# Optimization experiments

Hardware: AMD Instinct MI355X
Metric: run time of the kernel (lower is better)

Reference implementation:

```python
import jax, jax.numpy as jnp
import numpy as np

LN_EPS = 1e-5
NORM_EPS = 1e-12  # F.normalize eps


def _l2norm(x):
    # torch F.normalize(p=2, dim=-1): x / max(||x||, eps)
    n = jnp.sqrt(jnp.sum(x * x, axis=-1, keepdims=True))
    return x / jnp.maximum(n, NORM_EPS)


def setup_inputs() -> dict:
    key = jax.random.key(0)
    D, R, H = 256, 32, 64  # d_model, rank, d_model//4
    B, C, P = 32, 64, 96
    ks = jax.random.split(key, 16)
    s = 0.05
    return {
        "x": jax.random.normal(ks[0], (B * C, P, D), jnp.float32),
        "ln_gamma": jnp.ones((D,), jnp.float32),
        "ln_beta": jnp.zeros((D,), jnp.float32),
        "Wd": jax.random.normal(ks[1], (D, R), jnp.float32) * s,
        "bd": jax.random.normal(ks[2], (R,), jnp.float32) * s,
        "Wq": jax.random.normal(ks[3], (R, R), jnp.float32) * s,
        "Wk": jax.random.normal(ks[4], (R, R), jnp.float32) * s,
        "Wv": jax.random.normal(ks[5], (R, R), jnp.float32) * s,
        "Wg": jax.random.normal(ks[6], (R, R), jnp.float32) * s,
        "bg": jax.random.normal(ks[7], (R,), jnp.float32) * s,
        "Wu": jax.random.normal(ks[8], (R, D), jnp.float32) * s,
        "bu": jax.random.normal(ks[9], (D,), jnp.float32) * s,
        "W1": jax.random.normal(ks[10], (D, H), jnp.float32) * s,
        "b1": jax.random.normal(ks[11], (H,), jnp.float32) * s,
        "W2": jax.random.normal(ks[12], (H, D), jnp.float32) * s,
        "b2": jnp.full((D,), -5.0, jnp.float32),  # gate_init bias
        "B": B,
        "C": C,
    }


def reference(x, ln_gamma, ln_beta, Wd, bd, Wq, Wk, Wv, Wg, bg, Wu, bu, W1, b1, W2, b2, B, C):
    BC, P, D = x.shape
    # [B*C, P, D] -> [B*P, C, D] channel-mixing layout
    h = x.reshape(B, C, P, D).transpose(0, 2, 1, 3).reshape(B * P, C, D)

    # LayerNorm over D (biased variance, as in torch LayerNorm)
    mu = jnp.mean(h, axis=-1, keepdims=True)
    var = jnp.var(h, axis=-1, keepdims=True)
    h_norm = (h - mu) * jax.lax.rsqrt(var + LN_EPS) * ln_gamma + ln_beta

    # bottleneck projection to rank R
    h_low = h_norm @ Wd + bd  # [BP, C, R]

    # Hydra linear attention: cosine-normalized Q/K, sum-pooled K*V global feature
    Q = _l2norm(h_low @ Wq)
    K = _l2norm(h_low @ Wk)
    V = h_low @ Wv
    global_feat = jnp.sum(K * V, axis=1, keepdims=True)  # [BP, 1, R]
    h_attn = Q * global_feat

    # content gate and up-projection
    gate_c = jax.nn.sigmoid(h_low @ Wg + bg)
    mixed = (h_attn * gate_c) @ Wu + bu  # [BP, C, D]

    # AdaptiveGate: unbiased variance over channel dim (torch .var default ddof=1)
    chan_var = jnp.var(h, axis=1, ddof=1)  # [BP, D]
    gate_logits = jax.nn.gelu(chan_var @ W1 + b1, approximate=False) @ W2 + b2
    gate = jax.nn.sigmoid(gate_logits)[:, None, :]  # [BP, 1, D]

    out = h + gate * mixed
    # back to [B*C, P, D]
    return out.reshape(B, P, C, D).transpose(0, 2, 1, 3).reshape(BC, P, D)
```

## Files before the change

### kernel.cpp

```cpp
#include <hip/hip_runtime.h>
#include <hip/hip_bf16.h>

#define DD 256
#define RR 32
#define CC 64
#define PB 96
#define NT 1024

typedef __attribute__((ext_vector_type(8))) short short8;
typedef __attribute__((ext_vector_type(4))) float f32x4;

__device__ __forceinline__ short f2bf(float f) {
    return __builtin_bit_cast(short, __float2bfloat16(f));
}
__device__ __forceinline__ float b2f(unsigned short s) {
    union { unsigned u; float f; } v; v.u = ((unsigned)s) << 16;
    return v.f;
}

__device__ __forceinline__ int hswz(int c, int d) {
    return c * 256 + (d ^ ((c & 7) << 3));
}
__device__ __forceinline__ int nswz(int r, int k) {
    return r * 32 + (k ^ (((r >> 1) & 3) << 3));
}

__global__ __launch_bounds__(1024, 1)
void prep_kernel(const float* __restrict__ ln_g, const float* __restrict__ ln_b,
                 const float* __restrict__ Wd, const float* __restrict__ bd,
                 const float* __restrict__ Wq, const float* __restrict__ Wk,
                 const float* __restrict__ Wv, const float* __restrict__ Wg,
                 const float* __restrict__ Wu,
                 const float* __restrict__ W1, const float* __restrict__ W2,
                 short* __restrict__ wsWd, short* __restrict__ wsQKVG,
                 short* __restrict__ wsWu, float* __restrict__ wsLN,
                 float* __restrict__ wsW1T, float* __restrict__ wsW2T)
{
    __shared__ float redp[2048];
    const int t = threadIdx.x;
    {
        const int r = t >> 5, dblk = t & 31;
        short8 vv;
        float sa = 0.f, sb = 0.f;
        #pragma unroll
        for (int j = 0; j < 8; ++j) {
            const int d = dblk * 8 + j;
            const float wd = Wd[d * RR + r];
            const float g  = ln_g[d];
            vv[j] = f2bf(g * wd);
            sa += g * wd;
            sb += ln_b[d] * wd;
        }
        *(short8*)&wsWd[r * 256 + ((dblk ^ (r & 7)) << 3)] = vv;
        redp[r * 32 + dblk]        = sa;
        redp[1024 + r * 32 + dblk] = sb;
    }
    if (t < 512) {
        const int m = t >> 7, rr2 = (t >> 2) & 31, kg = t & 3;
        const float* Wm = (m == 0) ? Wq : (m == 1) ? Wk : (m == 2) ? Wv : Wg;
        short8 vv;
        #pragma unroll
        for (int j = 0; j < 8; ++j)
            vv[j] = f2bf(Wm[(kg * 8 + j) * RR + rr2]);
        *(short8*)&wsQKVG[m * 1024 + rr2 * 32 + ((kg ^ ((rr2 >> 1) & 3)) << 3)] = vv;
    }
    {
        const int d = t & 255, kg = t >> 8;
        short8 vv;
        #pragma unroll
        for (int j = 0; j < 8; ++j)
            vv[j] = f2bf(Wu[(kg * 8 + j) * DD + d]);
        *(short8*)&wsWu[d * 32 + ((kg ^ ((d >> 1) & 3)) << 3)] = vv;
    }
    #pragma unroll
    for (int rep = 0; rep < 16; ++rep) {
        const int id = rep * 1024 + t;
        const int j = id >> 8, d = id & 255;
        wsW1T[j * 256 + d] = W1[d * 64 + j];
    }
    #pragma unroll
    for (int rep = 0; rep < 16; ++rep) {
        const int id = rep * 1024 + t;
        const int d = id >> 6, j = id & 63;
        wsW2T[d * 64 + j] = W2[j * 256 + d];
    }
    __syncthreads();
    if (t < 32) {
        float s = 0.f;
        #pragma unroll
        for (int g = 0; g < 32; ++g) s += redp[t * 32 + g];
        wsLN[t] = s;
    } else if (t < 64) {
        const int r = t - 32;
        float s = 0.f;
        #pragma unroll
        for (int g = 0; g < 32; ++g) s += redp[1024 + r * 32 + g];
        wsLN[t] = s + bd[r];
    }
}

__global__ __launch_bounds__(NT, 8)
void hydra_kernel(const float* __restrict__ x,
                  const short* __restrict__ wsWd, const short* __restrict__ wsQKVG,
                  const short* __restrict__ wsWu, const float* __restrict__ wsLN,
                  const float* __restrict__ wsW1T, const float* __restrict__ wsW2T,
                  const float* __restrict__ bg,
                  const float* __restrict__ bu,
                  const float* __restrict__ b1, const float* __restrict__ b2,
                  float* __restrict__ out)
{
    __shared__ short hbf[CC * DD];
    __shared__ short wreg[RR * DD];
    __shared__ short qg[CC * RR];
    __shared__ short lowbuf[CC * RR];
    __shared__ float redA[1024];
    __shared__ float redB[2048];
    __shared__ float redC[1024];
    __shared__ float mu_s[CC], rstd_s[CC];
    __shared__ float cv_s[DD], gate_s[DD];
    __shared__ float hid_s[64];
    __shared__ float ln_a[RR], ln_bv[RR];

    const int t    = threadIdx.x;
    const int lane = t & 63;
    const int w    = t >> 6;
    const int bp   = blockIdx.x;
    const int b    = bp / PB;
    const int p    = bp - b * PB;
    const size_t rowbase = (size_t)(b * CC) * PB * DD + (size_t)p * DD;

    #pragma unroll
    for (int i = 0; i < 4; ++i) {
        const int c = w * 4 + i;
        const float4 v = *(const float4*)(x + rowbase + (size_t)c * (PB * DD) + 4 * lane);
        float s1 = v.x + v.y + v.z + v.w;
        float s2 = v.x * v.x + v.y * v.y + v.z * v.z + v.w * v.w;
        s1 += __shfl_xor(s1, 1, 64); s2 += __shfl_xor(s2, 1, 64);
        s1 += __shfl_xor(s1, 2, 64); s2 += __shfl_xor(s2, 2, 64);
        s1 += __shfl_xor(s1, 4, 64); s2 += __shfl_xor(s2, 4, 64);
        if ((lane & 7) == 0)
            *(float2*)&redC[(c * 8 + (lane >> 3)) * 2] = make_float2(s1, s2);
        ushort4 pk;
        pk.x = (unsigned short)f2bf(v.x); pk.y = (unsigned short)f2bf(v.y);
        pk.z = (unsigned short)f2bf(v.z); pk.w = (unsigned short)f2bf(v.w);
        *(ushort4*)&hbf[hswz(c, 4 * lane)] = pk;
    }
    *(short8*)&wreg[t * 8] = *(const short8*)&wsWd[t * 8];
    if (t < 32)              ln_a[t]       = wsLN[t];
    else if (t < 64)         ln_bv[t - 32] = wsLN[t];
    __syncthreads();

    f32x4 s3acc = {0.f, 0.f, 0.f, 0.f};
    if (w < 8) {
        const int ct = w >> 1, rt = w & 1;
        const int arow = ct * 16 + (lane & 15);
        const int brow = rt * 16 + (lane & 15);
        const int ksub = lane >> 4;
        #pragma unroll
        for (int step = 0; step < 8; ++step) {
            const short8 a  = *(const short8*)&hbf[hswz(arow, step * 32 + ksub * 8)];
            const short8 bf = *(const short8*)&wreg[hswz(brow, step * 32 + ksub * 8)];
            s3acc = __builtin_amdgcn_mfma_f32_16x16x32_bf16(a, bf, s3acc, 0, 0, 0);
        }
    } else {
        const int idx = t - 512;
        const int dp  = idx & 127;
        const int rg  = idx >> 7;
        const int d0  = dp * 2;
        float s1a = 0.f, s1b = 0.f, s2a = 0.f, s2b = 0.f;
        #pragma unroll
        for (int i = 0; i < 16; ++i) {
            const int c = rg * 16 + i;
            const ushort2 u = *(const ushort2*)&hbf[hswz(c, d0)];
            const float va = b2f(u.x), vb = b2f(u.y);
            s1a += va; s2a += va * va;
            s1b += vb; s2b += vb * vb;
        }
        *(float2*)&redB[rg * 256 + d0]        = make_float2(s1a, s1b);
        *(float2*)&redB[1024 + rg * 256 + d0] = make_float2(s2a, s2b);
        if (idx < 64) {
            const int c = idx;
            float s1 = 0.f, s2 = 0.f;
            #pragma unroll
            for (int g = 0; g < 8; ++g) {
                const float2 pr = *(const float2*)&redC[(c * 8 + g) * 2];
                s1 += pr.x; s2 += pr.y;
            }
            const float mu = s1 * (1.f / 256.f);
            mu_s[c]   = mu;
            rstd_s[c] = rsqrtf(s2 * (1.f / 256.f) - mu * mu + 1e-5f);
        }
    }
    __syncthreads();

    if (w < 8) {
        const int ct = w >> 1, rt = w & 1;
        const int col = rt * 16 + (lane & 15);
        const float la = ln_a[col], lb = ln_bv[col];
        #pragma unroll
        for (int i = 0; i < 4; ++i) {
            const int c = ct * 16 + (lane >> 4) * 4 + i;
            const float rs = rstd_s[c];
            const float hl = rs * s3acc[i] - rs * mu_s[c] * la + lb;
            lowbuf[nswz(c, col)] = f2bf(hl);
        }
    } else {
        const int idx = t - 512;
        *(short8*)&wreg[idx * 8] = *(const short8*)&wsQKVG[idx * 8];
    }
    if (t < 256) {
        const float S1 = redB[t] + redB[256 + t] + redB[512 + t] + redB[768 + t];
        const float S2 = redB[1024 + t] + redB[1280 + t] + redB[1536 + t] + redB[1792 + t];
        cv_s[t] = (S2 - S1 * S1 * (1.f / 64.f)) * (1.f / 63.f);
    }
    __syncthreads();

    if (w < 8) {
        const int ct = w >> 1, pair = w & 1;
        const int mA = pair ? 1 : 0;
        const int mB = pair ? 2 : 3;
        const int arow = ct * 16 + (lane & 15);
        const int ksub = lane >> 4;
        const short8 a = *(const short8*)&lowbuf[nswz(arow, ksub * 8)];
        f32x4 aA0 = {0,0,0,0}, aA1 = {0,0,0,0}, aB0 = {0,0,0,0}, aB1 = {0,0,0,0};
        {
            const int br0 = (lane & 15), br1 = 16 + (lane & 15);
            const short8 bA0 = *(const short8*)&wreg[mA * 1024 + nswz(br0, ksub * 8)];
            const short8 bA1 = *(const short8*)&wreg[mA * 1024 + nswz(br1, ksub * 8)];
            const short8 bB0 = *(const short8*)&wreg[mB * 1024 + nswz(br0, ksub * 8)];
            const short8 bB1 = *(const short8*)&wreg[mB * 1024 + nswz(br1, ksub * 8)];
            aA0 = __builtin_amdgcn_mfma_f32_16x16x32_bf16(a, bA0, aA0, 0, 0, 0);
            aA1 = __builtin_amdgcn_mfma_f32_16x16x32_bf16(a, bA1, aA1, 0, 0, 0);
            aB0 = __builtin_amdgcn_mfma_f32_16x16x32_bf16(a, bB0, aB0, 0, 0, 0);
            aB1 = __builtin_amdgcn_mfma_f32_16x16x32_bf16(a, bB1, aB1, 0, 0, 0);
        }
        float qs[4];
        #pragma unroll
        for (int i = 0; i < 4; ++i) {
            float ss = aA0[i] * aA0[i] + aA1[i] * aA1[i];
            ss += __shfl_xor(ss, 1, 64);
            ss += __shfl_xor(ss, 2, 64);
            ss += __shfl_xor(ss, 4, 64);
            ss += __shfl_xor(ss, 8, 64);
            qs[i] = 1.f / fmaxf(sqrtf(ss), 1e-12f);
        }
        const int col0 = (lane & 15), col1 = 16 + (lane & 15);
        if (pair == 0) {
            const float bgv0 = bg[col0], bgv1 = bg[col1];
            #pragma unroll
            for (int i = 0; i < 4; ++i) {
                const int c = ct * 16 + (lane >> 4) * 4 + i;
                const float g0 = 1.f / (1.f + __expf(-(aB0[i] + bgv0)));
                const float g1 = 1.f / (1.f + __expf(-(aB1[i] + bgv1)));
                qg[c * 32 + col0] = f2bf(aA0[i] * qs[i] * g0);
                qg[c * 32 + col1] = f2bf(aA1[i] * qs[i] * g1);
            }
        } else {
            #pragma unroll
            for (int i = 0; i < 4; ++i) {
                const int c = ct * 16 + (lane >> 4) * 4 + i;
                redB[c * 32 + col0] = aA0[i] * qs[i] * aB0[i];
                redB[c * 32 + col1] = aA1[i] * qs[i] * aB1[i];
            }
        }
    } else {
        const int idx = t - 512;
        const int j = idx & 63, dg = idx >> 6;
        const float* w1row = wsW1T + j * 256 + dg * 32;
        float s = 0.f;
        #pragma unroll
        for (int ii = 0; ii < 8; ++ii) {
            const float4 wv = *(const float4*)(w1row + ii * 4);
            const float4 cvv = *(const float4*)&cv_s[dg * 32 + ii * 4];
            s += cvv.x * wv.x + cvv.y * wv.y + cvv.z * wv.z + cvv.w * wv.w;
        }
        redA[dg * 64 + j] = s;
    }
    __syncthreads();

    if (t < 64) {
        float s = b1[t];
        #pragma unroll
        for (int g = 0; g < 8; ++g) s += redA[g * 64 + t];
        hid_s[t] = 0.5f * s * (1.f + erff(s * 0.70710678118654752f));
    }
    if (t >= 256 && t < 512) {
        const int idx = t - 256;
        const int r = idx & 31, g = idx >> 5;
        float s = 0.f;
        #pragma unroll
        for (int i = 0; i < 8; ++i)
            s += redB[(g * 8 + i) * 32 + r];
        redA[512 + g * 32 + r] = s;
    }
    *(short8*)&wreg[t * 8] = *(const short8*)&wsWu[t * 8];
    __syncthreads();

    {
        const int d = t & 255, jg = t >> 8;
        const float* w2row = wsW2T + d * 64 + jg * 16;
        float s = 0.f;
        #pragma unroll
        for (int ii = 0; ii < 4; ++ii) {
            const float4 wv = *(const float4*)(w2row + ii * 4);
            const float4 hv = *(const float4*)&hid_s[jg * 16 + ii * 4];
            s += hv.x * wv.x + hv.y * wv.y + hv.z * wv.z + hv.w * wv.w;
        }
        redB[jg * 256 + d] = s;
    }
    if (t < 256) {
        const int r = t & 31, c0 = t >> 5, c1 = (t >> 5) + 32;
        float gf = 0.f;
        #pragma unroll
        for (int g = 0; g < 8; ++g) gf += redA[512 + g * 32 + r];
        lowbuf[nswz(c0, r)] = f2bf(b2f((unsigned short)qg[c0 * 32 + r]) * gf);
        lowbuf[nswz(c1, r)] = f2bf(b2f((unsigned short)qg[c1 * 32 + r]) * gf);
    }
    __syncthreads();

    {
        const int ct = w & 3, dg = w >> 2;
        const int arow = ct * 16 + (lane & 15);
        const int ksub = lane >> 4;
        const short8 a = *(const short8*)&lowbuf[nswz(arow, ksub * 8)];
        #pragma unroll
        for (int j = 0; j < 4; ++j) {
            const int col = (dg * 4 + j) * 16 + (lane & 15);
            const short8 bf = *(const short8*)&wreg[nswz(col, ksub * 8)];
            f32x4 acc = {0.f, 0.f, 0.f, 0.f};
            acc = __builtin_amdgcn_mfma_f32_16x16x32_bf16(a, bf, acc, 0, 0, 0);
            #pragma unroll
            for (int i = 0; i < 4; ++i) {
                const int c = ct * 16 + (lane >> 4) * 4 + i;
                hbf[hswz(c, col)] = f2bf(acc[i]);
            }
        }
    }
    if (t < 256) {
        const float s = redB[t] + redB[256 + t] + redB[512 + t] + redB[768 + t] + b2[t];
        gate_s[t] = 1.f / (1.f + __expf(-s));
    }
    __syncthreads();

    #pragma unroll
    for (int i = 0; i < 4; ++i) {
        const int c = w * 4 + i;
        const size_t off = rowbase + (size_t)c * (PB * DD) + 4 * lane;
        const float4 xv = *(const float4*)(x + off);
        const ushort4 m = *(const ushort4*)&hbf[hswz(c, 4 * lane)];
        const float4 g4 = *(const float4*)&gate_s[4 * lane];
        const float4 bu4 = *(const float4*)(bu + 4 * lane);
        float4 o;
        o.x = xv.x + g4.x * (b2f(m.x) + bu4.x);
        o.y = xv.y + g4.y * (b2f(m.y) + bu4.y);
        o.z = xv.z + g4.z * (b2f(m.z) + bu4.z);
        o.w = xv.w + g4.w * (b2f(m.w) + bu4.w);
        *(float4*)(out + off) = o;
    }
}

extern "C" void kernel_launch(void* const* d_in, const int* in_sizes, int n_in,
                              void* d_out, int out_size, void* d_ws, size_t ws_size,
                              hipStream_t stream) {
    (void)in_sizes; (void)n_in; (void)out_size; (void)ws_size;
    const float* x    = (const float*)d_in[0];
    const float* ln_g = (const float*)d_in[1];
    const float* ln_b = (const float*)d_in[2];
    const float* Wd   = (const float*)d_in[3];
    const float* bd   = (const float*)d_in[4];
    const float* Wq   = (const float*)d_in[5];
    const float* Wk   = (const float*)d_in[6];
    const float* Wv   = (const float*)d_in[7];
    const float* Wg   = (const float*)d_in[8];
    const float* bg   = (const float*)d_in[9];
    const float* Wu   = (const float*)d_in[10];
    const float* bu   = (const float*)d_in[11];
    const float* W1   = (const float*)d_in[12];
    const float* b1   = (const float*)d_in[13];
    const float* W2   = (const float*)d_in[14];
    const float* b2   = (const float*)d_in[15];
    float* out = (float*)d_out;

    short* wsWd   = (short*)d_ws;
    short* wsQKVG = wsWd + 8192;
    short* wsWu   = wsQKVG + 4096;
    float* wsLN   = (float*)(wsWd + 20480);
    float* wsW1T  = wsLN + 64;
    float* wsW2T  = wsW1T + 16384;

    prep_kernel<<<dim3(1), dim3(1024), 0, stream>>>(
        ln_g, ln_b, Wd, bd, Wq, Wk, Wv, Wg, Wu, W1, W2,
        wsWd, wsQKVG, wsWu, wsLN, wsW1T, wsW2T);
    hydra_kernel<<<dim3(32 * PB), dim3(NT), 0, stream>>>(
        x, wsWd, wsQKVG, wsWu, wsLN, wsW1T, wsW2T, bg, bu, b1, b2, out);
}
```

Before: 169.7 us.

## Pre-pack weights into MFMA fragment order and load B operands from global

The prep kernel now writes Wd, Wq/Wk/Wv/Wg and Wu in per-lane MFMA fragment order. The main kernel reads each B operand with one coalesced short8 global load instead of staging the weights through a 16KB shared buffer. This removes the shared weight buffer and its staging copies and cuts LDS use per block, which may allow more resident blocks. The cost is repeated global/L2 reads of the weights by every block. Those reads should be cache-resident but add latency inside the MFMA loops.

```diff
diff --git a/kernel.cpp b/kernel.cpp
--- a/kernel.cpp
+++ b/kernel.cpp
@@ -32,45 +32,60 @@
                  const float* __restrict__ Wv, const float* __restrict__ Wg,
                  const float* __restrict__ Wu,
                  const float* __restrict__ W1, const float* __restrict__ W2,
-                 short* __restrict__ wsWd, short* __restrict__ wsQKVG,
-                 short* __restrict__ wsWu, float* __restrict__ wsLN,
+                 short* __restrict__ wsF1, short* __restrict__ wsF2,
+                 short* __restrict__ wsF3, float* __restrict__ wsLN,
                  float* __restrict__ wsW1T, float* __restrict__ wsW2T)
 {
     __shared__ float redp[2048];
     const int t = threadIdx.x;
     {
         const int r = t >> 5, dblk = t & 31;
-        short8 vv;
         float sa = 0.f, sb = 0.f;
         #pragma unroll
         for (int j = 0; j < 8; ++j) {
             const int d = dblk * 8 + j;
             const float wd = Wd[d * RR + r];
-            const float g  = ln_g[d];
-            vv[j] = f2bf(g * wd);
-            sa += g * wd;
+            sa += ln_g[d] * wd;
             sb += ln_b[d] * wd;
         }
-        *(short8*)&wsWd[r * 256 + ((dblk ^ (r & 7)) << 3)] = vv;
         redp[r * 32 + dblk]        = sa;
         redp[1024 + r * 32 + dblk] = sb;
     }
+    {
+        const int f = t >> 6, l = t & 63;
+        const int rt = f >> 3, step = f & 7;
+        const int r = rt * 16 + (l & 15);
+        short8 v;
+        #pragma unroll
+        for (int j = 0; j < 8; ++j) {
+            const int d = step * 32 + (l >> 4) * 8 + j;
+            v[j] = f2bf(ln_g[d] * Wd[d * RR + r]);
+        }
+        *(short8*)&wsF1[f * 512 + l * 8] = v;
+    }
     if (t < 512) {
-        const int m = t >> 7, rr2 = (t >> 2) & 31, kg = t & 3;
+        const int f = t >> 6, l = t & 63;
+        const int m = f >> 1, half = f & 1;
         const float* Wm = (m == 0) ? Wq : (m == 1) ? Wk : (m == 2) ? Wv : Wg;
-        short8 vv;
-        #pragma unroll
-        for (int j = 0; j < 8; ++j)
-            vv[j] = f2bf(Wm[(kg * 8 + j) * RR + rr2]);
-        *(short8*)&wsQKVG[m * 1024 + rr2 * 32 + ((kg ^ ((rr2 >> 1) & 3)) << 3)] = vv;
+        const int rout = half * 16 + (l & 15);
+        short8 v;
+        #pragma unroll
+        for (int j = 0; j < 8; ++j) {
+            const int rin = (l >> 4) * 8 + j;
+            v[j] = f2bf(Wm[rin * RR + rout]);
+        }
+        *(short8*)&wsF2[f * 512 + l * 8] = v;
     }
     {
-        const int d = t & 255, kg = t >> 8;
-        short8 vv;
-        #pragma unroll
-        for (int j = 0; j < 8; ++j)
-            vv[j] = f2bf(Wu[(kg * 8 + j) * DD + d]);
-        *(short8*)&wsWu[d * 32 + ((kg ^ ((d >> 1) & 3)) << 3)] = vv;
+        const int f = t >> 6, l = t & 63;
+        const int d = f * 16 + (l & 15);
+        short8 v;
+        #pragma unroll
+        for (int j = 0; j < 8; ++j) {
+            const int r = (l >> 4) * 8 + j;
+            v[j] = f2bf(Wu[r * DD + d]);
+        }
+        *(short8*)&wsF3[f * 512 + l * 8] = v;
     }
     #pragma unroll
     for (int rep = 0; rep < 16; ++rep) {
@@ -101,8 +116,8 @@
 
 __global__ __launch_bounds__(NT, 8)
 void hydra_kernel(const float* __restrict__ x,
-                  const short* __restrict__ wsWd, const short* __restrict__ wsQKVG,
-                  const short* __restrict__ wsWu, const float* __restrict__ wsLN,
+                  const short* __restrict__ wsF1, const short* __restrict__ wsF2,
+                  const short* __restrict__ wsF3, const float* __restrict__ wsLN,
                   const float* __restrict__ wsW1T, const float* __restrict__ wsW2T,
                   const float* __restrict__ bg,
                   const float* __restrict__ bu,
@@ -110,7 +125,6 @@
                   float* __restrict__ out)
 {
     __shared__ short hbf[CC * DD];
-    __shared__ short wreg[RR * DD];
     __shared__ short qg[CC * RR];
     __shared__ short lowbuf[CC * RR];
     __shared__ float redA[1024];
@@ -145,7 +159,6 @@
         pk.z = (unsigned short)f2bf(v.z); pk.w = (unsigned short)f2bf(v.w);
         *(ushort4*)&hbf[hswz(c, 4 * lane)] = pk;
     }
-    *(short8*)&wreg[t * 8] = *(const short8*)&wsWd[t * 8];
     if (t < 32)              ln_a[t]       = wsLN[t];
     else if (t < 64)         ln_bv[t - 32] = wsLN[t];
     __syncthreads();
@@ -154,12 +167,12 @@
     if (w < 8) {
         const int ct = w >> 1, rt = w & 1;
         const int arow = ct * 16 + (lane & 15);
-        const int brow = rt * 16 + (lane & 15);
-        const int ksub = lane >> 4;
+        const int kofs = (lane >> 4) * 8;
+        const short* fB = wsF1 + rt * 8 * 512 + lane * 8;
         #pragma unroll
         for (int step = 0; step < 8; ++step) {
-            const short8 a  = *(const short8*)&hbf[hswz(arow, step * 32 + ksub * 8)];
-            const short8 bf = *(const short8*)&wreg[hswz(brow, step * 32 + ksub * 8)];
+            const short8 bf = *(const short8*)(fB + step * 512);
+            const short8 a  = *(const short8*)&hbf[hswz(arow, step * 32 + kofs)];
             s3acc = __builtin_amdgcn_mfma_f32_16x16x32_bf16(a, bf, s3acc, 0, 0, 0);
         }
     } else {
@@ -204,14 +217,11 @@
             const float hl = rs * s3acc[i] - rs * mu_s[c] * la + lb;
             lowbuf[nswz(c, col)] = f2bf(hl);
         }
-    } else {
-        const int idx = t - 512;
-        *(short8*)&wreg[idx * 8] = *(const short8*)&wsQKVG[idx * 8];
-    }
-    if (t < 256) {
-        const float S1 = redB[t] + redB[256 + t] + redB[512 + t] + redB[768 + t];
-        const float S2 = redB[1024 + t] + redB[1280 + t] + redB[1536 + t] + redB[1792 + t];
-        cv_s[t] = (S2 - S1 * S1 * (1.f / 64.f)) * (1.f / 63.f);
+    } else if (t < 768) {
+        const int d = t - 512;
+        const float S1 = redB[d] + redB[256 + d] + redB[512 + d] + redB[768 + d];
+        const float S2 = redB[1024 + d] + redB[1280 + d] + redB[1536 + d] + redB[1792 + d];
+        cv_s[d] = (S2 - S1 * S1 * (1.f / 64.f)) * (1.f / 63.f);
     }
     __syncthreads();
 
@@ -220,20 +230,17 @@
         const int mA = pair ? 1 : 0;
         const int mB = pair ? 2 : 3;
         const int arow = ct * 16 + (lane & 15);
-        const int ksub = lane >> 4;
-        const short8 a = *(const short8*)&lowbuf[nswz(arow, ksub * 8)];
+        const int kofs = (lane >> 4) * 8;
+        const short8 a = *(const short8*)&lowbuf[nswz(arow, kofs)];
+        const short8 bA0 = *(const short8*)(wsF2 + (mA * 2 + 0) * 512 + lane * 8);
+        const short8 bA1 = *(const short8*)(wsF2 + (mA * 2 + 1) * 512 + lane * 8);
+        const short8 bB0 = *(const short8*)(wsF2 + (mB * 2 + 0) * 512 + lane * 8);
+        const short8 bB1 = *(const short8*)(wsF2 + (mB * 2 + 1) * 512 + lane * 8);
         f32x4 aA0 = {0,0,0,0}, aA1 = {0,0,0,0}, aB0 = {0,0,0,0}, aB1 = {0,0,0,0};
-        {
-            const int br0 = (lane & 15), br1 = 16 + (lane & 15);
-            const short8 bA0 = *(const short8*)&wreg[mA * 1024 + nswz(br0, ksub * 8)];
-            const short8 bA1 = *(const short8*)&wreg[mA * 1024 + nswz(br1, ksub * 8)];
-            const short8 bB0 = *(const short8*)&wreg[mB * 1024 + nswz(br0, ksub * 8)];
-            const short8 bB1 = *(const short8*)&wreg[mB * 1024 + nswz(br1, ksub * 8)];
-            aA0 = __builtin_amdgcn_mfma_f32_16x16x32_bf16(a, bA0, aA0, 0, 0, 0);
-            aA1 = __builtin_amdgcn_mfma_f32_16x16x32_bf16(a, bA1, aA1, 0, 0, 0);
-            aB0 = __builtin_amdgcn_mfma_f32_16x16x32_bf16(a, bB0, aB0, 0, 0, 0);
-            aB1 = __builtin_amdgcn_mfma_f32_16x16x32_bf16(a, bB1, aB1, 0, 0, 0);
-        }
+        aA0 = __builtin_amdgcn_mfma_f32_16x16x32_bf16(a, bA0, aA0, 0, 0, 0);
+        aA1 = __builtin_amdgcn_mfma_f32_16x16x32_bf16(a, bA1, aA1, 0, 0, 0);
+        aB0 = __builtin_amdgcn_mfma_f32_16x16x32_bf16(a, bB0, aB0, 0, 0, 0);
+        aB1 = __builtin_amdgcn_mfma_f32_16x16x32_bf16(a, bB1, aB1, 0, 0, 0);
         float qs[4];
         #pragma unroll
         for (int i = 0; i < 4; ++i) {
@@ -293,7 +300,6 @@
             s += redB[(g * 8 + i) * 32 + r];
         redA[512 + g * 32 + r] = s;
     }
-    *(short8*)&wreg[t * 8] = *(const short8*)&wsWu[t * 8];
     __syncthreads();
 
     {
@@ -321,12 +327,13 @@
     {
         const int ct = w & 3, dg = w >> 2;
         const int arow = ct * 16 + (lane & 15);
-        const int ksub = lane >> 4;
-        const short8 a = *(const short8*)&lowbuf[nswz(arow, ksub * 8)];
+        const int kofs = (lane >> 4) * 8;
+        const short8 a = *(const short8*)&lowbuf[nswz(arow, kofs)];
         #pragma unroll
         for (int j = 0; j < 4; ++j) {
-            const int col = (dg * 4 + j) * 16 + (lane & 15);
-            const short8 bf = *(const short8*)&wreg[nswz(col, ksub * 8)];
+            const int dt = dg * 4 + j;
+            const int col = dt * 16 + (lane & 15);
+            const short8 bf = *(const short8*)(wsF3 + dt * 512 + lane * 8);
             f32x4 acc = {0.f, 0.f, 0.f, 0.f};
             acc = __builtin_amdgcn_mfma_f32_16x16x32_bf16(a, bf, acc, 0, 0, 0);
             #pragma unroll
@@ -381,16 +388,16 @@
     const float* b2   = (const float*)d_in[15];
     float* out = (float*)d_out;
 
-    short* wsWd   = (short*)d_ws;
-    short* wsQKVG = wsWd + 8192;
-    short* wsWu   = wsQKVG + 4096;
-    float* wsLN   = (float*)(wsWd + 20480);
-    float* wsW1T  = wsLN + 64;
-    float* wsW2T  = wsW1T + 16384;
+    short* wsF1  = (short*)d_ws;
+    short* wsF2  = wsF1 + 8192;
+    short* wsF3  = wsF2 + 4096;
+    float* wsLN  = (float*)(wsF1 + 20480);
+    float* wsW1T = wsLN + 64;
+    float* wsW2T = wsW1T + 16384;
 
     prep_kernel<<<dim3(1), dim3(1024), 0, stream>>>(
         ln_g, ln_b, Wd, bd, Wq, Wk, Wv, Wg, Wu, W1, W2,
-        wsWd, wsQKVG, wsWu, wsLN, wsW1T, wsW2T);
+        wsF1, wsF2, wsF3, wsLN, wsW1T, wsW2T);
     hydra_kernel<<<dim3(32 * PB), dim3(NT), 0, stream>>>(
-        x, wsWd, wsQKVG, wsWu, wsLN, wsW1T, wsW2T, bg, bu, b1, b2, out);
-}
+        x, wsF1, wsF2, wsF3, wsLN, wsW1T, wsW2T, bg, bu, b1, b2, out);
+}
```

Result: no change. 171.4 us (+1.0%).

## Fuse gated residual epilogue into the up-projection MFMA and merge gate GEMV

Applied to the files above, without the earlier changes.

The W2 gate GEMV is now done by one thread per output column, bias and sigmoid included, in the same phase as the Q*global scaling. This removes the partial-sum reduction buffer and a barrier. The final output is now written straight from the MFMA accumulators, which removes the staging of mixed in shared memory, another barrier, and the second global read of x. The residual now comes from the bf16 copy of h held in shared memory instead of fp32 x, which lowers output precision. Stores become 16-wide scattered column writes instead of contiguous float4 rows, so write coalescing gets worse.

```diff
diff --git a/kernel.cpp b/kernel.cpp
--- a/kernel.cpp
+++ b/kernel.cpp
@@ -296,18 +296,6 @@
     *(short8*)&wreg[t * 8] = *(const short8*)&wsWu[t * 8];
     __syncthreads();
 
-    {
-        const int d = t & 255, jg = t >> 8;
-        const float* w2row = wsW2T + d * 64 + jg * 16;
-        float s = 0.f;
-        #pragma unroll
-        for (int ii = 0; ii < 4; ++ii) {
-            const float4 wv = *(const float4*)(w2row + ii * 4);
-            const float4 hv = *(const float4*)&hid_s[jg * 16 + ii * 4];
-            s += hv.x * wv.x + hv.y * wv.y + hv.z * wv.z + hv.w * wv.w;
-        }
-        redB[jg * 256 + d] = s;
-    }
     if (t < 256) {
         const int r = t & 31, c0 = t >> 5, c1 = (t >> 5) + 32;
         float gf = 0.f;
@@ -315,6 +303,17 @@
         for (int g = 0; g < 8; ++g) gf += redA[512 + g * 32 + r];
         lowbuf[nswz(c0, r)] = f2bf(b2f((unsigned short)qg[c0 * 32 + r]) * gf);
         lowbuf[nswz(c1, r)] = f2bf(b2f((unsigned short)qg[c1 * 32 + r]) * gf);
+    } else if (t < 512) {
+        const int d = t - 256;
+        const float* w2row = wsW2T + d * 64;
+        float s = b2[d];
+        #pragma unroll
+        for (int ii = 0; ii < 16; ++ii) {
+            const float4 wv = *(const float4*)(w2row + ii * 4);
+            const float4 hv = *(const float4*)&hid_s[ii * 4];
+            s += hv.x * wv.x + hv.y * wv.y + hv.z * wv.z + hv.w * wv.w;
+        }
+        gate_s[d] = 1.f / (1.f + __expf(-s));
     }
     __syncthreads();
 
@@ -329,33 +328,15 @@
             const short8 bf = *(const short8*)&wreg[nswz(col, ksub * 8)];
             f32x4 acc = {0.f, 0.f, 0.f, 0.f};
             acc = __builtin_amdgcn_mfma_f32_16x16x32_bf16(a, bf, acc, 0, 0, 0);
+            const float gt  = gate_s[col];
+            const float buv = bu[col];
             #pragma unroll
             for (int i = 0; i < 4; ++i) {
                 const int c = ct * 16 + (lane >> 4) * 4 + i;
-                hbf[hswz(c, col)] = f2bf(acc[i]);
+                const float xv = b2f((unsigned short)hbf[hswz(c, col)]);
+                out[rowbase + (size_t)c * (PB * DD) + col] = xv + gt * (acc[i] + buv);
             }
         }
-    }
-    if (t < 256) {
-        const float s = redB[t] + redB[256 + t] + redB[512 + t] + redB[768 + t] + b2[t];
-        gate_s[t] = 1.f / (1.f + __expf(-s));
-    }
-    __syncthreads();
-
-    #pragma unroll
-    for (int i = 0; i < 4; ++i) {
-        const int c = w * 4 + i;
-        const size_t off = rowbase + (size_t)c * (PB * DD) + 4 * lane;
-        const float4 xv = *(const float4*)(x + off);
-        const ushort4 m = *(const ushort4*)&hbf[hswz(c, 4 * lane)];
-        const float4 g4 = *(const float4*)&gate_s[4 * lane];
-        const float4 bu4 = *(const float4*)(bu + 4 * lane);
-        float4 o;
-        o.x = xv.x + g4.x * (b2f(m.x) + bu4.x);
-        o.y = xv.y + g4.y * (b2f(m.y) + bu4.y);
-        o.z = xv.z + g4.z * (b2f(m.z) + bu4.z);
-        o.w = xv.w + g4.w * (b2f(m.w) + bu4.w);
-        *(float4*)(out + off) = o;
     }
 }
 
```

After: 163.1 us. 3.9% less time.
